# Kernel tuning notes

Hardware: AMD Instinct MI355X
Metric: run time of the kernel (lower is better)

The kernel has to match this reference:

```python
import jax, jax.numpy as jnp
import numpy as np

IN_FEATURES = 512
OUT_FEATURES = 512
GRID_SIZE = 8
BATCH = 4096


def setup_inputs() -> dict:
    key = jax.random.key(0)
    k_x, k_sw, k_ba = jax.random.split(key, 3)
    x = jax.random.normal(k_x, (BATCH, IN_FEATURES), dtype=jnp.float32)
    spline_weight = jax.random.normal(k_sw, (OUT_FEATURES, IN_FEATURES, GRID_SIZE), dtype=jnp.float32)
    base_activation = jax.random.normal(k_ba, (OUT_FEATURES, IN_FEATURES), dtype=jnp.float32)
    grid_points = jnp.linspace(-1.0, 1.0, GRID_SIZE, dtype=jnp.float32)
    return {"x": x, "spline_weight": spline_weight, "base_activation": base_activation, "grid_points": grid_points}


def _bspline_basis(d):
    # piecewise cubic: d = |x - grid|
    inner = 1.0 - 6.0 * d * d + 6.0 * d * d * d
    outer = 2.0 * (1.0 - d) ** 3
    return jnp.where(d < 0.5, inner, jnp.where(d < 1.0, outer, jnp.zeros_like(d)))


def reference(x, spline_weight, base_activation, grid_points):
    x_norm = jnp.tanh(x)                                  # (B, in)
    d = jnp.abs(x_norm[:, :, None] - grid_points)          # (B, in, grid)
    basis = _bspline_basis(d)                              # (B, in, grid)
    # sum over grid then in_features, weighted by spline_weight (out, in, grid)
    spline_out = jnp.einsum('big,oig->bo', basis, spline_weight)
    base_out = x_norm @ base_activation.T                  # (B, out)
    return spline_out + 0.1 * base_out
```

## Files before the change

### kernel.cpp

```cpp
#include <hip/hip_runtime.h>

#define IN_F   512
#define OUT_F  512
#define GRID_N 8
#define BATCH  4096
#define KDIM   (IN_F * 9)
#define SPLITK 4
#define KCHUNK (KDIM / SPLITK)
#define BK     64
#define BKSTEPS (KCHUNK / BK)

typedef __fp16 half8 __attribute__((ext_vector_type(8)));
typedef float  f32x4 __attribute__((ext_vector_type(4)));

__device__ __forceinline__ void gload16(const void* gsrc, void* ldst) {
  __builtin_amdgcn_global_load_lds(
      (__attribute__((address_space(1))) void*)(void*)gsrc,
      (__attribute__((address_space(3))) void*)ldst, 16, 0, 0);
}

__global__ void prep_kernel(const float* __restrict__ x, const float* __restrict__ grid,
                            const float* __restrict__ sw, const float* __restrict__ ba,
                            __fp16* __restrict__ A, __fp16* __restrict__ W) {
  const int bid = blockIdx.x;
  if (bid < (BATCH * IN_F) / 256) {
    const int idx = bid * 256 + threadIdx.x;
    const float xn = tanhf(x[idx]);
    const int b = idx >> 9;
    const int i = idx & (IN_F - 1);
    __fp16* arow = A + (size_t)b * KDIM + i;
#pragma unroll
    for (int g = 0; g < GRID_N; ++g) {
      const float d  = fabsf(xn - grid[g]);
      const float dd = d * d;
      const float inner = 1.0f - 6.0f * dd + 6.0f * dd * d;
      const float om = 1.0f - d;
      const float outer = 2.0f * om * om * om;
      const float bas = (d < 0.5f) ? inner : ((d < 1.0f) ? outer : 0.0f);
      arow[g * IN_F] = (__fp16)bas;
    }
    arow[8 * IN_F] = (__fp16)xn;
  } else {
    const int idx = (bid - (BATCH * IN_F) / 256) * 256 + threadIdx.x;
    const float* swp = sw + (size_t)idx * GRID_N;
    __fp16* wrow = W + (size_t)(idx >> 9) * KDIM + (idx & (IN_F - 1));
#pragma unroll
    for (int g = 0; g < GRID_N; ++g) wrow[g * IN_F] = (__fp16)swp[g];
    wrow[8 * IN_F] = (__fp16)(0.1f * ba[idx]);
  }
}

__global__ __launch_bounds__(256) void gemm_kernel(const __fp16* __restrict__ A,
                                                   const __fp16* __restrict__ W,
                                                   float* __restrict__ P) {
  __shared__ __align__(16) __fp16 As[128 * BK];
  __shared__ __align__(16) __fp16 Bs[128 * BK];
  const int tid  = threadIdx.x;
  const int lane = tid & 63;
  const int wv   = tid >> 6;
  const int wm   = wv >> 1;
  const int wn   = wv & 1;
  const int m0 = blockIdx.x * 128;
  const int n0 = blockIdx.y * 128;
  const int kbase = blockIdx.z * KCHUNK;

  const __fp16* Ag[4];
  const __fp16* Wg[4];
  __fp16* lA[4];
  __fp16* lB[4];
#pragma unroll
  for (int j = 0; j < 4; ++j) {
    const int t = wv * 4 + j;
    const int r = t * 8 + (lane >> 3);
    const int cs = (((lane & 7) ^ (r & 7))) * 8;
    Ag[j] = A + (size_t)(m0 + r) * KDIM + kbase + cs;
    Wg[j] = W + (size_t)(n0 + r) * KDIM + kbase + cs;
    lA[j] = &As[t * 512];
    lB[j] = &Bs[t * 512];
  }

  const int fr = lane & 15;
  const int g4 = lane >> 4;
  const int xr = fr & 7;

  f32x4 acc[4][4] = {};

  for (int kt = 0; kt < BKSTEPS; ++kt) {
#pragma unroll
    for (int j = 0; j < 4; ++j) {
      gload16(Ag[j], lA[j]);
      gload16(Wg[j], lB[j]);
      Ag[j] += BK; Wg[j] += BK;
    }
    __syncthreads();

    half8 a[2][4], b[2][4];
#pragma unroll
    for (int ks = 0; ks < 2; ++ks) {
#pragma unroll
      for (int mi = 0; mi < 4; ++mi) {
        const int row = wm * 64 + mi * 16 + fr;
        const int ch = (ks * 4 + g4) ^ xr;
        a[ks][mi] = *(const half8*)&As[row * BK + ch * 8];
      }
#pragma unroll
      for (int ni = 0; ni < 4; ++ni) {
        const int row = wn * 64 + ni * 16 + fr;
        const int ch = (ks * 4 + g4) ^ xr;
        b[ks][ni] = *(const half8*)&Bs[row * BK + ch * 8];
      }
    }
#pragma unroll
    for (int ks = 0; ks < 2; ++ks)
#pragma unroll
      for (int mi = 0; mi < 4; ++mi)
#pragma unroll
        for (int ni = 0; ni < 4; ++ni)
          acc[mi][ni] = __builtin_amdgcn_mfma_f32_16x16x32_f16(a[ks][mi], b[ks][ni], acc[mi][ni], 0, 0, 0);
    __syncthreads();
  }

  float* Pp = P + (size_t)blockIdx.z * (BATCH * OUT_F);
#pragma unroll
  for (int mi = 0; mi < 4; ++mi) {
#pragma unroll
    for (int ni = 0; ni < 4; ++ni) {
      const int row = m0 + wm * 64 + mi * 16 + g4 * 4;
      const int col = n0 + wn * 64 + ni * 16 + fr;
#pragma unroll
      for (int rg = 0; rg < 4; ++rg)
        Pp[(size_t)(row + rg) * OUT_F + col] = acc[mi][ni][rg];
    }
  }
}

__global__ void reduce_kernel(const float* __restrict__ P, float* __restrict__ out) {
  const int idx = blockIdx.x * 256 + threadIdx.x;
  const f32x4* P4 = (const f32x4*)P;
  const int stride = (BATCH * OUT_F) / 4;
  f32x4 s = P4[idx] + P4[idx + stride] + P4[idx + 2 * stride] + P4[idx + 3 * stride];
  ((f32x4*)out)[idx] = s;
}

extern "C" void kernel_launch(void* const* d_in, const int* in_sizes, int n_in,
                              void* d_out, int out_size, void* d_ws, size_t ws_size,
                              hipStream_t stream) {
  const float* x  = (const float*)d_in[0];
  const float* sw = (const float*)d_in[1];
  const float* ba = (const float*)d_in[2];
  const float* gp = (const float*)d_in[3];
  float* out = (float*)d_out;

  char* ws = (char*)d_ws;
  const size_t A_BYTES = (size_t)BATCH * KDIM * 2;
  const size_t W_BYTES = (size_t)OUT_F * KDIM * 2;
  __fp16* A = (__fp16*)ws;
  __fp16* W = (__fp16*)(ws + A_BYTES);
  float*  P = (float*)(ws + A_BYTES + W_BYTES);

  const int FEAT_BLKS = (BATCH * IN_F) / 256;
  const int WT_BLKS   = (OUT_F * IN_F) / 256;
  prep_kernel<<<FEAT_BLKS + WT_BLKS, 256, 0, stream>>>(x, gp, sw, ba, A, W);
  gemm_kernel<<<dim3(BATCH / 128, OUT_F / 128, SPLITK), 256, 0, stream>>>(A, W, P);
  reduce_kernel<<<(BATCH * OUT_F) / 4 / 256, 256, 0, stream>>>(P, out);
}
```

Measured before the change: 109.4 us.

## Double-buffer LDS and enlarge GEMM tile to 128x256 with 512 threads

Restructures the split-K GEMM to use a 128x256 block tile with 8 waves (512 threads), double-buffered LDS, and a flattened 1D grid that groups the N and split-K blocks sharing the same M rows. The next K-tile's global-to-LDS loads are issued before computing on the current tile, and one barrier per iteration replaces two. This is meant to overlap memory latency with MFMA work and raise reuse of each loaded A tile. In exchange LDS use grows to 96KB per block, which may limit occupancy, and the block count halves.

```diff
diff --git a/kernel.cpp b/kernel.cpp
--- a/kernel.cpp
+++ b/kernel.cpp
@@ -7,8 +7,10 @@
 #define KDIM   (IN_F * 9)
 #define SPLITK 4
 #define KCHUNK (KDIM / SPLITK)
-#define BK     64
-#define BKSTEPS (KCHUNK / BK)
+#define BM 128
+#define BN 256
+#define BK 64
+#define NSTEPS (KCHUNK / BK)
 
 typedef __fp16 half8 __attribute__((ext_vector_type(8)));
 typedef float  f32x4 __attribute__((ext_vector_type(4)));
@@ -50,77 +52,87 @@
   }
 }
 
-__global__ __launch_bounds__(256) void gemm_kernel(const __fp16* __restrict__ A,
-                                                   const __fp16* __restrict__ W,
-                                                   float* __restrict__ P) {
-  __shared__ __align__(16) __fp16 As[128 * BK];
-  __shared__ __align__(16) __fp16 Bs[128 * BK];
+__global__ __launch_bounds__(512, 2) void gemm_kernel(const __fp16* __restrict__ A,
+                                                      const __fp16* __restrict__ W,
+                                                      float* __restrict__ P) {
+  __shared__ __align__(16) __fp16 As[2][BM * BK];
+  __shared__ __align__(16) __fp16 Bs[2][BN * BK];
   const int tid  = threadIdx.x;
   const int lane = tid & 63;
+  const int fr   = lane & 15;
+  const int g4   = lane >> 4;
   const int wv   = tid >> 6;
-  const int wm   = wv >> 1;
-  const int wn   = wv & 1;
-  const int m0 = blockIdx.x * 128;
-  const int n0 = blockIdx.y * 128;
-  const int kbase = blockIdx.z * KCHUNK;
+  const int wm   = wv >> 2;
+  const int wn   = wv & 3;
+  const int wg   = blockIdx.x;
+  const int nz   = wg & 7;
+  const int mb   = wg >> 3;
+  const int m0   = mb * BM;
+  const int n0   = (nz & 1) * BN;
+  const int kbase = (nz >> 1) * KCHUNK;
 
-  const __fp16* Ag[4];
-  const __fp16* Wg[4];
-  __fp16* lA[4];
-  __fp16* lB[4];
+  const __fp16* Ag[2];
+  const __fp16* Bg[4];
+  int lAoff[2], lBoff[4];
+#pragma unroll
+  for (int j = 0; j < 2; ++j) {
+    const int c = j * 512 + tid;
+    const int r = c >> 3;
+    const int cc = (c & 7) ^ (r & 7);
+    Ag[j] = A + (size_t)(m0 + r) * KDIM + kbase + cc * 8;
+    lAoff[j] = c * 8;
+  }
 #pragma unroll
   for (int j = 0; j < 4; ++j) {
-    const int t = wv * 4 + j;
-    const int r = t * 8 + (lane >> 3);
-    const int cs = (((lane & 7) ^ (r & 7))) * 8;
-    Ag[j] = A + (size_t)(m0 + r) * KDIM + kbase + cs;
-    Wg[j] = W + (size_t)(n0 + r) * KDIM + kbase + cs;
-    lA[j] = &As[t * 512];
-    lB[j] = &Bs[t * 512];
+    const int c = j * 512 + tid;
+    const int r = c >> 3;
+    const int cc = (c & 7) ^ (r & 7);
+    Bg[j] = W + (size_t)(n0 + r) * KDIM + kbase + cc * 8;
+    lBoff[j] = c * 8;
   }
-
-  const int fr = lane & 15;
-  const int g4 = lane >> 4;
-  const int xr = fr & 7;
 
   f32x4 acc[4][4] = {};
 
-  for (int kt = 0; kt < BKSTEPS; ++kt) {
 #pragma unroll
-    for (int j = 0; j < 4; ++j) {
-      gload16(Ag[j], lA[j]);
-      gload16(Wg[j], lB[j]);
-      Ag[j] += BK; Wg[j] += BK;
+  for (int j = 0; j < 2; ++j) gload16(Ag[j], &As[0][lAoff[j]]);
+#pragma unroll
+  for (int j = 0; j < 4; ++j) gload16(Bg[j], &Bs[0][lBoff[j]]);
+
+  int cur = 0;
+  for (int kt = 0; kt < NSTEPS; ++kt) {
+    __syncthreads();
+    if (kt + 1 < NSTEPS) {
+      const int koff = (kt + 1) * BK;
+#pragma unroll
+      for (int j = 0; j < 2; ++j) gload16(Ag[j] + koff, &As[cur ^ 1][lAoff[j]]);
+#pragma unroll
+      for (int j = 0; j < 4; ++j) gload16(Bg[j] + koff, &Bs[cur ^ 1][lBoff[j]]);
     }
-    __syncthreads();
-
-    half8 a[2][4], b[2][4];
 #pragma unroll
     for (int ks = 0; ks < 2; ++ks) {
+      half8 a[4], b[4];
 #pragma unroll
       for (int mi = 0; mi < 4; ++mi) {
         const int row = wm * 64 + mi * 16 + fr;
-        const int ch = (ks * 4 + g4) ^ xr;
-        a[ks][mi] = *(const half8*)&As[row * BK + ch * 8];
+        const int ch = (ks * 4 + g4) ^ (fr & 7);
+        a[mi] = *(const half8*)&As[cur][row * BK + ch * 8];
       }
 #pragma unroll
       for (int ni = 0; ni < 4; ++ni) {
         const int row = wn * 64 + ni * 16 + fr;
-        const int ch = (ks * 4 + g4) ^ xr;
-        b[ks][ni] = *(const half8*)&Bs[row * BK + ch * 8];
+        const int ch = (ks * 4 + g4) ^ (fr & 7);
+        b[ni] = *(const half8*)&Bs[cur][row * BK + ch * 8];
       }
-    }
-#pragma unroll
-    for (int ks = 0; ks < 2; ++ks)
 #pragma unroll
       for (int mi = 0; mi < 4; ++mi)
 #pragma unroll
         for (int ni = 0; ni < 4; ++ni)
-          acc[mi][ni] = __builtin_amdgcn_mfma_f32_16x16x32_f16(a[ks][mi], b[ks][ni], acc[mi][ni], 0, 0, 0);
-    __syncthreads();
+          acc[mi][ni] = __builtin_amdgcn_mfma_f32_16x16x32_f16(a[mi], b[ni], acc[mi][ni], 0, 0, 0);
+    }
+    cur ^= 1;
   }
 
-  float* Pp = P + (size_t)blockIdx.z * (BATCH * OUT_F);
+  float* Pp = P + (size_t)(nz >> 1) * (BATCH * OUT_F);
 #pragma unroll
   for (int mi = 0; mi < 4; ++mi) {
 #pragma unroll
@@ -161,6 +173,6 @@
   const int FEAT_BLKS = (BATCH * IN_F) / 256;
   const int WT_BLKS   = (OUT_F * IN_F) / 256;
   prep_kernel<<<FEAT_BLKS + WT_BLKS, 256, 0, stream>>>(x, gp, sw, ba, A, W);
-  gemm_kernel<<<dim3(BATCH / 128, OUT_F / 128, SPLITK), 256, 0, stream>>>(A, W, P);
+  gemm_kernel<<<(BATCH / BM) * (OUT_F / BN) * SPLITK, 512, 0, stream>>>(A, W, P);
   reduce_kernel<<<(BATCH * OUT_F) / 4 / 256, 256, 0, stream>>>(P, out);
 }
```

Result: slower. 115.1 us (+5.2%).

## Double split-K, store fp16 partials, remap grid to 1D with launch bounds

Applied to the files above, without the earlier changes.

Raises split-K from 4 to 8, giving 1024 workgroups instead of 512 for more parallelism across CUs. The partial sums are now written as fp16 rather than fp32, which halves partial-buffer traffic, and the reduce kernel sums eight fp16 slices into fp32. The grid becomes 1D with the split index in the low bits, so neighbouring workgroups share the same A/W tile region, and launch bounds request 3 blocks per CU. Rounding partials to fp16 loses precision and could overflow, since the sums over 576 products of normal-distributed weights can be large.

```diff
diff --git a/kernel.cpp b/kernel.cpp
--- a/kernel.cpp
+++ b/kernel.cpp
@@ -5,10 +5,10 @@
 #define GRID_N 8
 #define BATCH  4096
 #define KDIM   (IN_F * 9)
-#define SPLITK 4
+#define SPLITK 8
 #define KCHUNK (KDIM / SPLITK)
 #define BK     64
-#define BKSTEPS (KCHUNK / BK)
+#define NSTEPS (KCHUNK / BK)
 
 typedef __fp16 half8 __attribute__((ext_vector_type(8)));
 typedef float  f32x4 __attribute__((ext_vector_type(4)));
@@ -50,9 +50,9 @@
   }
 }
 
-__global__ __launch_bounds__(256) void gemm_kernel(const __fp16* __restrict__ A,
-                                                   const __fp16* __restrict__ W,
-                                                   float* __restrict__ P) {
+__global__ __launch_bounds__(256, 3) void gemm_kernel(const __fp16* __restrict__ A,
+                                                      const __fp16* __restrict__ W,
+                                                      __fp16* __restrict__ P) {
   __shared__ __align__(16) __fp16 As[128 * BK];
   __shared__ __align__(16) __fp16 Bs[128 * BK];
   const int tid  = threadIdx.x;
@@ -60,9 +60,12 @@
   const int wv   = tid >> 6;
   const int wm   = wv >> 1;
   const int wn   = wv & 1;
-  const int m0 = blockIdx.x * 128;
-  const int n0 = blockIdx.y * 128;
-  const int kbase = blockIdx.z * KCHUNK;
+  const int wg   = blockIdx.x;
+  const int z    = wg & 7;
+  const int t    = wg >> 3;
+  const int m0   = (t >> 2) * 128;
+  const int n0   = (t & 3) * 128;
+  const int kbase = z * KCHUNK;
 
   const __fp16* Ag[4];
   const __fp16* Wg[4];
@@ -70,13 +73,13 @@
   __fp16* lB[4];
 #pragma unroll
   for (int j = 0; j < 4; ++j) {
-    const int t = wv * 4 + j;
-    const int r = t * 8 + (lane >> 3);
-    const int cs = (((lane & 7) ^ (r & 7))) * 8;
+    const int t4 = wv * 4 + j;
+    const int r = t4 * 8 + (lane >> 3);
+    const int cs = ((lane & 7) ^ (r & 7)) * 8;
     Ag[j] = A + (size_t)(m0 + r) * KDIM + kbase + cs;
     Wg[j] = W + (size_t)(n0 + r) * KDIM + kbase + cs;
-    lA[j] = &As[t * 512];
-    lB[j] = &Bs[t * 512];
+    lA[j] = &As[t4 * 512];
+    lB[j] = &Bs[t4 * 512];
   }
 
   const int fr = lane & 15;
@@ -85,7 +88,7 @@
 
   f32x4 acc[4][4] = {};
 
-  for (int kt = 0; kt < BKSTEPS; ++kt) {
+  for (int kt = 0; kt < NSTEPS; ++kt) {
 #pragma unroll
     for (int j = 0; j < 4; ++j) {
       gload16(Ag[j], lA[j]);
@@ -116,11 +119,12 @@
       for (int mi = 0; mi < 4; ++mi)
 #pragma unroll
         for (int ni = 0; ni < 4; ++ni)
+          acc[ks ? 1 : 0][0] = acc[ks ? 1 : 0][0],
           acc[mi][ni] = __builtin_amdgcn_mfma_f32_16x16x32_f16(a[ks][mi], b[ks][ni], acc[mi][ni], 0, 0, 0);
     __syncthreads();
   }
 
-  float* Pp = P + (size_t)blockIdx.z * (BATCH * OUT_F);
+  __fp16* Pp = P + (size_t)z * (BATCH * OUT_F);
 #pragma unroll
   for (int mi = 0; mi < 4; ++mi) {
 #pragma unroll
@@ -129,17 +133,24 @@
       const int col = n0 + wn * 64 + ni * 16 + fr;
 #pragma unroll
       for (int rg = 0; rg < 4; ++rg)
-        Pp[(size_t)(row + rg) * OUT_F + col] = acc[mi][ni][rg];
+        Pp[(size_t)(row + rg) * OUT_F + col] = (__fp16)acc[mi][ni][rg];
     }
   }
 }
 
-__global__ void reduce_kernel(const float* __restrict__ P, float* __restrict__ out) {
+__global__ void reduce_kernel(const __fp16* __restrict__ P, float* __restrict__ out) {
   const int idx = blockIdx.x * 256 + threadIdx.x;
-  const f32x4* P4 = (const f32x4*)P;
-  const int stride = (BATCH * OUT_F) / 4;
-  f32x4 s = P4[idx] + P4[idx + stride] + P4[idx + 2 * stride] + P4[idx + 3 * stride];
-  ((f32x4*)out)[idx] = s;
+  float s[8] = {};
+#pragma unroll
+  for (int zz = 0; zz < SPLITK; ++zz) {
+    const half8 v = *(const half8*)&P[(size_t)zz * (BATCH * OUT_F) + (size_t)idx * 8];
+#pragma unroll
+    for (int e = 0; e < 8; ++e) s[e] += (float)v[e];
+  }
+  f32x4 lo = {s[0], s[1], s[2], s[3]};
+  f32x4 hi = {s[4], s[5], s[6], s[7]};
+  ((f32x4*)out)[idx * 2]     = lo;
+  ((f32x4*)out)[idx * 2 + 1] = hi;
 }
 
 extern "C" void kernel_launch(void* const* d_in, const int* in_sizes, int n_in,
@@ -156,11 +167,11 @@
   const size_t W_BYTES = (size_t)OUT_F * KDIM * 2;
   __fp16* A = (__fp16*)ws;
   __fp16* W = (__fp16*)(ws + A_BYTES);
-  float*  P = (float*)(ws + A_BYTES + W_BYTES);
+  __fp16* P = (__fp16*)(ws + A_BYTES + W_BYTES);
 
   const int FEAT_BLKS = (BATCH * IN_F) / 256;
   const int WT_BLKS   = (OUT_F * IN_F) / 256;
   prep_kernel<<<FEAT_BLKS + WT_BLKS, 256, 0, stream>>>(x, gp, sw, ba, A, W);
-  gemm_kernel<<<dim3(BATCH / 128, OUT_F / 128, SPLITK), 256, 0, stream>>>(A, W, P);
-  reduce_kernel<<<(BATCH * OUT_F) / 4 / 256, 256, 0, stream>>>(P, out);
+  gemm_kernel<<<(BATCH / 128) * (OUT_F / 128) * SPLITK, 256, 0, stream>>>(A, W, P);
+  reduce_kernel<<<(BATCH * OUT_F) / 8 / 256, 256, 0, stream>>>(P, out);
 }
```

Result: faster. 106.9 us (-2.3%).
